# Kernel tuning notes

Hardware: AMD Instinct MI355X
Metric: run time of the kernel (lower is better)

## Reference

```python
import jax, jax.numpy as jnp
import numpy as np

B, T, F_IN, NF, K, H, NOUT = 512, 800, 3, 128, 15, 150, 10
EPS = 1e-5


def hard_sigmoid(x):
    # Keras-style hard sigmoid used by LSTMHardSigmoid gates
    return jnp.clip(0.2 * x + 0.5, 0.0, 1.0)


def adabn(x, gamma, beta, axes):
    # AdaBN: normalize with current-batch statistics, then learned affine.
    m = jnp.mean(x, axis=axes, keepdims=True)
    v = jnp.var(x, axis=axes, keepdims=True)
    shape = [1] * x.ndim
    shape[1] = x.shape[1]
    return (x - m) * jax.lax.rsqrt(v + EPS) * gamma.reshape(shape) + beta.reshape(shape)


def lstm_dir(x_tbf, w_ih, w_hh, b_ih, b_hh):
    # x_tbf: (T', B, F). PyTorch gate order i, f, g, o; hard-sigmoid gates.
    pre = jnp.einsum('tbf,gf->tbg', x_tbf, w_ih) + b_ih + b_hh  # (T', B, 4H)
    bsz = x_tbf.shape[1]
    h0 = jnp.zeros((bsz, H), x_tbf.dtype)
    c0 = jnp.zeros((bsz, H), x_tbf.dtype)

    def step(carry, pre_t):
        h, c = carry
        gates = pre_t + h @ w_hh.T
        i, f, g, o = jnp.split(gates, 4, axis=-1)
        i = hard_sigmoid(i)
        f = hard_sigmoid(f)
        o = hard_sigmoid(o)
        g = jnp.tanh(g)
        c = f * c + i * g
        h = o * jnp.tanh(c)
        return (h, c), h

    _, hs = jax.lax.scan(step, (h0, c0), pre)
    return hs  # (T', B, H)


def setup_inputs() -> dict:
    key = jax.random.key(0)
    ks = jax.random.split(key, 12)
    s = lambda i, shape, sc=0.05: jax.random.normal(ks[i], shape, jnp.float32) * sc
    G = 4 * H
    return {
        'x': jax.random.normal(ks[0], (B, F_IN, T), jnp.float32),
        'conv_w': s(1, (NF, F_IN, K)),
        'conv_b': jnp.zeros((NF,), jnp.float32),
        'bn1_g': jnp.ones((NF,), jnp.float32),
        'bn1_b': jnp.zeros((NF,), jnp.float32),
        'w_ih_f': s(2, (G, NF)), 'w_hh_f': s(3, (G, H)),
        'b_ih_f': jnp.zeros((G,), jnp.float32), 'b_hh_f': jnp.zeros((G,), jnp.float32),
        'w_ih_b': s(4, (G, NF)), 'w_hh_b': s(5, (G, H)),
        'b_ih_b': jnp.zeros((G,), jnp.float32), 'b_hh_b': jnp.zeros((G,), jnp.float32),
        'bn2_g': jnp.ones((2 * H,), jnp.float32), 'bn2_b': jnp.zeros((2 * H,), jnp.float32),
        'fc1_w': s(6, (50, 2 * H)), 'fc1_b': jnp.zeros((50,), jnp.float32),
        'bn3_g': jnp.ones((50,), jnp.float32), 'bn3_b': jnp.zeros((50,), jnp.float32),
        'fc2_w': s(7, (NOUT, 50)), 'fc2_b': jnp.zeros((NOUT,), jnp.float32),
    }


def reference(x, conv_w, conv_b, bn1_g, bn1_b,
              w_ih_f, w_hh_f, b_ih_f, b_hh_f,
              w_ih_b, w_hh_b, b_ih_b, b_hh_b,
              bn2_g, bn2_b, fc1_w, fc1_b, bn3_g, bn3_b, fc2_w, fc2_b):
    # net1: Conv1d(3->128, k=15) + ReLU + (Dropout=identity in eval) + MaxPool1d(2)
    y = jax.lax.conv_general_dilated(x, conv_w, (1,), 'VALID',
                                     dimension_numbers=('NCH', 'OIH', 'NCH'))
    y = jax.nn.relu(y + conv_b[None, :, None])  # (B, 128, 786)
    L = y.shape[2] // 2
    y = y[:, :, :2 * L].reshape(y.shape[0], NF, L, 2).max(-1)  # (B, 128, 393)
    # net1_adabn (per-channel over batch and time)
    y = adabn(y, bn1_g, bn1_b, axes=(0, 2))
    # net2: bidirectional hard-sigmoid LSTM, batch_first; zero initial states
    seq = jnp.transpose(y, (2, 0, 1))  # (393, B, 128)
    h_f = lstm_dir(seq, w_ih_f, w_hh_f, b_ih_f, b_hh_f)
    h_b = lstm_dir(seq[::-1], w_ih_b, w_hh_b, b_ih_b, b_hh_b)[::-1]
    h = jnp.concatenate([h_f, h_b], axis=-1)  # (393, B, 300)
    # global max-pool over time (F.max_pool1d with kernel = full length)
    pooled = h.max(axis=0)  # (B, 300)
    z = adabn(pooled, bn2_g, bn2_b, axes=(0,))
    z = jax.nn.relu(z @ fc1_w.T + fc1_b)  # (B, 50)
    z = adabn(z, bn3_g, bn3_b, axes=(0,))
    logits = z @ fc2_w.T + fc2_b  # (B, 10)
    return jax.nn.softmax(logits, axis=1)
```

## Files before the change

kernel.cpp:

```cpp
#include <hip/hip_runtime.h>
#include <math.h>

#define B_   512
#define T_   800
#define FIN  3
#define NF   128
#define KW   15
#define HID  150
#define LOUT 393
#define G4   600
#define NPAD 640
#define EPS  1e-5f

#define NT_  38
#define KT_  5
#define HSTR 152
#define PNT  40
#define PKT  4
#define PSTR 648

typedef _Float16 half8 __attribute__((ext_vector_type(8)));
typedef _Float16 half4 __attribute__((ext_vector_type(4)));
typedef float f32x4 __attribute__((ext_vector_type(4)));

__device__ __forceinline__ float hsig(float x){ return fminf(fmaxf(0.2f*x+0.5f,0.f),1.f); }
__device__ __forceinline__ float ftanh(float x){ float e=__expf(2.f*x); return 1.f - 2.f/(e+1.f); }

__global__ __launch_bounds__(512) void k_conv2(const float* __restrict__ x,
        const float* __restrict__ cw, const float* __restrict__ cb,
        _Float16* __restrict__ y16, float* __restrict__ st){
  __shared__ float xs[FIN][800];
  __shared__ float wl[NF*FIN*KW];
  __shared__ float rs[4][128], rq[4][128];
  int tid = threadIdx.x;
  int b = blockIdx.x;
  for (int i=tid;i<FIN*800;i+=512) (&xs[0][0])[i] = x[(size_t)b*(FIN*T_) + i];
  for (int i=tid;i<NF*FIN*KW;i+=512) wl[i]=cw[i];
  __syncthreads();
  int c = tid & 127, li = tid >> 7;
  float wr[FIN*KW];
  #pragma unroll
  for (int i=0;i<FIN*KW;i++) wr[i]=wl[c*FIN*KW+i];
  float cbv = cb[c];
  float s=0.f, q=0.f;
  for (int l=li; l<LOUT; l+=4){
    float a0=0.f, a1=0.f;
    #pragma unroll
    for (int f=0;f<FIN;f++){
      const float2* xp = (const float2*)&xs[f][0] + l;
      float xv[16];
      #pragma unroll
      for (int p=0;p<8;p++){ float2 v=xp[p]; xv[2*p]=v.x; xv[2*p+1]=v.y; }
      #pragma unroll
      for (int k=0;k<KW;k++){ float w=wr[f*KW+k]; a0 += w*xv[k]; a1 += w*xv[k+1]; }
    }
    float v = fmaxf(fmaxf(a0,a1)+cbv, 0.f);
    y16[((size_t)b*LOUT + l)*NF + c] = (_Float16)v;
    s += v; q += v*v;
  }
  rs[li][c]=s; rq[li][c]=q;
  __syncthreads();
  if (tid < 128){
    float ts = rs[0][c]+rs[1][c]+rs[2][c]+rs[3][c];
    float tq = rq[0][c]+rq[1][c]+rq[2][c]+rq[3][c];
    atomicAdd(&st[c], ts);
    atomicAdd(&st[128+c], tq);
  }
}

__global__ void k_prep_bias(const float* __restrict__ st,
    const float* __restrict__ g1, const float* __restrict__ b1v,
    const float* __restrict__ wf, const float* __restrict__ wb,
    const float* __restrict__ bif, const float* __restrict__ bhf,
    const float* __restrict__ bib, const float* __restrict__ bhb,
    float* __restrict__ bef, float* __restrict__ beb){
  int id = blockIdx.x*256 + threadIdx.x;
  if (id >= 2*NPAD) return;
  int dir = id/NPAD, g = id%NPAD;
  float* be = dir? beb : bef;
  if (g >= G4){ be[g]=0.f; return; }
  int src = (g&3)*HID + (g>>2);
  const float* wih = dir? wb : wf;
  float bias = dir? (bib[src]+bhb[src]) : (bif[src]+bhf[src]);
  const float Ninv = 1.f/((float)B_*(float)LOUT);
  for (int f=0;f<NF;f++){
    float m = st[f]*Ninv;
    float var = st[NF+f]*Ninv - m*m;
    float a = g1[f]*rsqrtf(var+EPS);
    float d = b1v[f] - m*a;
    bias += d*wih[(size_t)src*NF+f];
  }
  be[g] = bias;
}

__global__ void k_prep_wih(const float* __restrict__ st,
    const float* __restrict__ g1,
    const float* __restrict__ wf, const float* __restrict__ wb,
    _Float16* __restrict__ wT16){
  int id = blockIdx.x*256 + threadIdx.x;
  if (id >= 2*PNT*PKT*64) return;
  int lane = id & 63;
  int kt = (id>>6) & 3;
  int nt = (id>>8) % PNT;
  int dir = id / (PNT*PKT*64);
  const float* wih = dir? wb : wf;
  int n = nt*16 + (lane&15);
  int src = (n&3)*HID + (n>>2);
  int kb = kt*32 + (lane>>4)*8;
  const float Ninv = 1.f/((float)B_*(float)LOUT);
  half8 v;
  #pragma unroll
  for (int j=0;j<8;j++){
    int k = kb+j;
    float m = st[k]*Ninv;
    float var = st[NF+k]*Ninv - m*m;
    float a = g1[k]*rsqrtf(var+EPS);
    float f = (n < G4) ? wih[(size_t)src*NF + k]*a : 0.f;
    v[j] = (_Float16)f;
  }
  *(half8*)&wT16[(size_t)id*8] = v;
}

__global__ void k_prep_whh(const float* __restrict__ whf, const float* __restrict__ whb,
                           _Float16* __restrict__ wfrag){
  int id = blockIdx.x*256 + threadIdx.x;
  if (id >= 2*NT_*KT_*64) return;
  int lane = id & 63;
  int rest = id >> 6;
  int kt = rest % KT_;
  int nt = (rest/KT_) % NT_;
  int dir = rest / (KT_*NT_);
  const float* wh = dir? whb : whf;
  int n = nt*16 + (lane&15);
  int src = (n&3)*HID + (n>>2);
  int kb = kt*32 + (lane>>4)*8;
  half8 v;
  #pragma unroll
  for (int j=0;j<8;j++){
    int k = kb + j;
    float f = (n < G4 && k < HID) ? wh[(size_t)src*HID + k] : 0.f;
    v[j] = (_Float16)f;
  }
  *(half8*)&wfrag[(size_t)id*8] = v;
}

__global__ __launch_bounds__(1024)
void k_mega(const _Float16* __restrict__ wfrag,
            const _Float16* __restrict__ wT16,
            const float* __restrict__ bef, const float* __restrict__ beb,
            const _Float16* __restrict__ y16,
            const _Float16* __restrict__ prf, const _Float16* __restrict__ prb,
            _Float16* __restrict__ pwf, _Float16* __restrict__ pwb,
            float* __restrict__ hst, float* __restrict__ cst, float* __restrict__ mst,
            float* __restrict__ pooled,
            int nrec, int tc, int first, int last, int t0p){
  __shared__ __align__(16) _Float16 hh[2][16][168];
  __shared__ __align__(16) _Float16 pls[2][16][PSTR];
  int tid = threadIdx.x;
  int bid = blockIdx.x;

  if (bid < nrec){
    int dir = bid >> 5;
    int b0 = (bid & 31) * 16;
    const _Float16* pre = dir? prb : prf;
    int lane = tid & 63, w = tid >> 6;

    int cnt  = (w<6) ? 3 : 2;
    int base = (w<6) ? 3*w : 18 + 2*(w-6);
    const _Float16* wf = wfrag + (size_t)dir*NT_*KT_*64*8;
    half8 bfr[3][5];
    #pragma unroll
    for (int i=0;i<3;i++){
      #pragma unroll
      for (int kt=0;kt<KT_;kt++){
        int ntc = (i<cnt)? (base+i) : base;
        bfr[i][kt] = *(const half8*)&wf[(size_t)((ntc*KT_+kt)*64 + lane)*8];
      }
    }

    int batch = lane & 15;
    int uo[3]; bool uv[3];
    #pragma unroll
    for (int i=0;i<3;i++){
      uo[i] = (base+i)*4 + (lane>>4);
      uv[i] = (i<cnt) && (uo[i] < HID);
    }

    int srow0 = tid/80,        scol0 = (tid%80)*8;
    int srow1 = (tid+1024)/80, scol1 = ((tid+1024)%80)*8;
    bool s2 = tid < 256;

    for (int i=tid; i<2*16*168; i+=1024) (&hh[0][0][0])[i] = (_Float16)0.f;
    float c[3], m[3], hl[3];
    #pragma unroll
    for (int i=0;i<3;i++){ c[i]=0.f; m[i]=-1e30f; hl[i]=0.f; }
    __syncthreads();
    if (!first){
      #pragma unroll
      for (int i=0;i<3;i++){
        if (uv[i]){
          size_t gi = ((size_t)(dir*B_ + b0 + batch))*HSTR + uo[i];
          c[i]=cst[gi]; m[i]=mst[gi]; hl[i]=hst[gi];
          hh[0][batch][uo[i]] = (_Float16)hl[i];
        }
      }
    }
    {
      half8 s0 = *(const half8*)(pre + ((size_t)(b0 + srow0))*NPAD + scol0);
      *(half8*)&pls[0][srow0][scol0] = s0;
      if (s2){
        half8 s1 = *(const half8*)(pre + ((size_t)(b0 + srow1))*NPAD + scol1);
        *(half8*)&pls[0][srow1][scol1] = s1;
      }
    }
    __syncthreads();

    int cur = 0;
    for (int t=0; t<tc; t++){
      int nxt = cur ^ 1;
      half8 s0, s1;
      bool ld = (t+1 < tc);
      if (ld){
        size_t rbase = (size_t)(t+1)*B_ + b0;
        s0 = *(const half8*)(pre + (rbase + srow0)*NPAD + scol0);
        if (s2) s1 = *(const half8*)(pre + (rbase + srow1)*NPAD + scol1);
      }
      f32x4 acc0={0,0,0,0}, acc1={0,0,0,0}, acc2={0,0,0,0};
      #pragma unroll
      for (int kt=0; kt<KT_; kt++){
        half8 a = *(const half8*)&hh[cur][batch][kt*32 + (lane>>4)*8];
        acc0 = __builtin_amdgcn_mfma_f32_16x16x32_f16(bfr[0][kt], a, acc0, 0,0,0);
        acc1 = __builtin_amdgcn_mfma_f32_16x16x32_f16(bfr[1][kt], a, acc1, 0,0,0);
        if (cnt>2) acc2 = __builtin_amdgcn_mfma_f32_16x16x32_f16(bfr[2][kt], a, acc2, 0,0,0);
      }
      #define CELL(ACC, I)                                                     \
      if (uv[I]){                                                              \
        half4 pv = *(const half4*)&pls[cur][batch][4*uo[I]];                   \
        float xi = ACC[0] + (float)pv[0];                                      \
        float xf = ACC[1] + (float)pv[1];                                      \
        float xg = ACC[2] + (float)pv[2];                                      \
        float xo = ACC[3] + (float)pv[3];                                      \
        float ig=hsig(xi), fg=hsig(xf), og=hsig(xo), gg=ftanh(xg);             \
        c[I] = fg*c[I] + ig*gg;                                                \
        float hv = og*ftanh(c[I]);                                             \
        m[I] = fmaxf(m[I], hv);                                                \
        hl[I] = hv;                                                            \
        hh[nxt][batch][uo[I]] = (_Float16)hv;                                  \
      }
      CELL(acc0, 0)
      CELL(acc1, 1)
      CELL(acc2, 2)
      #undef CELL
      if (ld){
        *(half8*)&pls[nxt][srow0][scol0] = s0;
        if (s2) *(half8*)&pls[nxt][srow1][scol1] = s1;
      }
      __syncthreads();
      cur = nxt;
    }

    #pragma unroll
    for (int i=0;i<3;i++){
      if (uv[i]){
        size_t gi = ((size_t)(dir*B_ + b0 + batch))*HSTR + uo[i];
        cst[gi]=c[i]; mst[gi]=m[i]; hst[gi]=hl[i];
        if (last) pooled[(size_t)(b0+batch)*300 + dir*HID + uo[i]] = m[i];
      }
    }
    return;
  }

  {
    int pb = bid - nrec;
    int dir  = pb & 1;
    int t5   = pb >> 1;
    int by   = t5 % 5;
    int t2   = t5 / 5;
    int mb   = t2 & 1;
    int trel = t2 >> 1;
    const _Float16* wfp = wT16 + (size_t)dir*PNT*PKT*64*8;
    const float* be = dir? beb : bef;
    _Float16* pre = dir? pwb : pwf;
    int t = dir ? (LOUT-1-t0p-trel) : (t0p+trel);
    int n0 = by*128, nb = n0>>4;
    int lane = tid & 63, ww = tid >> 6;
    int m0 = mb*256 + ww*16;
    int arow = lane&15, aq = (lane>>4)*8;
    const _Float16* ap = y16 + ((size_t)(m0+arow)*LOUT + t)*NF + aq;
    f32x4 acc[8];
    #pragma unroll
    for (int j=0;j<8;j++) acc[j] = (f32x4){0,0,0,0};
    #pragma unroll
    for (int kt=0; kt<PKT; kt++){
      half8 a = *(const half8*)(ap + kt*32);
      #pragma unroll
      for (int nt=0; nt<8; nt++){
        half8 bf = *(const half8*)&wfp[(size_t)(((nb+nt)*PKT + kt)*64 + lane)*8];
        acc[nt] = __builtin_amdgcn_mfma_f32_16x16x32_f16(a, bf, acc[nt], 0,0,0);
      }
    }
    int dcol = lane&15, dq = (lane>>4)*4;
    size_t rowg = (size_t)trel*B_ + m0 + dq;
    #pragma unroll
    for (int nt=0; nt<8; nt++){
      int colL = n0 + nt*16 + dcol;
      float bv = be[colL];
      #pragma unroll
      for (int r=0;r<4;r++)
        pre[(rowg+r)*NPAD + colL] = (_Float16)(acc[nt][r] + bv);
    }
  }
}

__global__ void k_stats2(const float* __restrict__ pooled,
    const float* __restrict__ g2, const float* __restrict__ b2,
    float* __restrict__ a2, float* __restrict__ d2){
  int f = threadIdx.x;
  if (f >= 300) return;
  float s=0.f,q=0.f;
  for (int b=0;b<B_;b++){ float v = pooled[(size_t)b*300+f]; s+=v; q+=v*v; }
  float m = s*(1.f/B_), var = q*(1.f/B_) - m*m;
  float a = g2[f]*rsqrtf(var+EPS);
  a2[f]=a; d2[f]=b2[f]-m*a;
}

__global__ void k_fc1(const float* __restrict__ pooled,
    const float* __restrict__ a2, const float* __restrict__ d2,
    const float* __restrict__ w1, const float* __restrict__ fb1,
    float* __restrict__ z1){
  int o = blockIdx.x*256 + threadIdx.x;
  if (o >= B_*50) return;
  int b = o/50, j = o%50;
  float acc = fb1[j];
  for (int f=0;f<300;f++)
    acc += (a2[f]*pooled[(size_t)b*300+f] + d2[f]) * w1[j*300+f];
  z1[o] = fmaxf(acc,0.f);
}

__global__ void k_stats3(const float* __restrict__ z1,
    const float* __restrict__ g3, const float* __restrict__ b3,
    float* __restrict__ a3, float* __restrict__ d3){
  int f = threadIdx.x;
  if (f >= 50) return;
  float s=0.f,q=0.f;
  for (int b=0;b<B_;b++){ float v = z1[(size_t)b*50+f]; s+=v; q+=v*v; }
  float m = s*(1.f/B_), var = q*(1.f/B_) - m*m;
  float a = g3[f]*rsqrtf(var+EPS);
  a3[f]=a; d3[f]=b3[f]-m*a;
}

__global__ void k_fc2(const float* __restrict__ z1,
    const float* __restrict__ a3, const float* __restrict__ d3,
    const float* __restrict__ w2, const float* __restrict__ fb2,
    float* __restrict__ out){
  int b = blockIdx.x;
  int t = threadIdx.x;
  __shared__ float zl[50];
  __shared__ float lg[10];
  if (t<50) zl[t] = a3[t]*z1[(size_t)b*50+t] + d3[t];
  __syncthreads();
  if (t<10){
    float acc = fb2[t];
    for (int j=0;j<50;j++) acc += zl[j]*w2[t*50+j];
    lg[t]=acc;
  }
  __syncthreads();
  if (t<10){
    float m = lg[0];
    #pragma unroll
    for (int i=1;i<10;i++) m = fmaxf(m,lg[i]);
    float s = 0.f;
    #pragma unroll
    for (int i=0;i<10;i++) s += expf(lg[i]-m);
    out[(size_t)b*10+t] = expf(lg[t]-m)/s;
  }
}

extern "C" void kernel_launch(void* const* d_in, const int* in_sizes, int n_in,
                              void* d_out, int out_size, void* d_ws, size_t ws_size,
                              hipStream_t stream) {
  const float* x    = (const float*)d_in[0];
  const float* cw   = (const float*)d_in[1];
  const float* cb   = (const float*)d_in[2];
  const float* g1   = (const float*)d_in[3];
  const float* b1v  = (const float*)d_in[4];
  const float* wihf = (const float*)d_in[5];
  const float* whhf = (const float*)d_in[6];
  const float* bihf = (const float*)d_in[7];
  const float* bhhf = (const float*)d_in[8];
  const float* wihb = (const float*)d_in[9];
  const float* whhb = (const float*)d_in[10];
  const float* bihb = (const float*)d_in[11];
  const float* bhhb = (const float*)d_in[12];
  const float* g2   = (const float*)d_in[13];
  const float* b2   = (const float*)d_in[14];
  const float* w1   = (const float*)d_in[15];
  const float* fb1  = (const float*)d_in[16];
  const float* g3   = (const float*)d_in[17];
  const float* b3   = (const float*)d_in[18];
  const float* w2   = (const float*)d_in[19];
  const float* fb2  = (const float*)d_in[20];
  float* out = (float*)d_out;

  uint8_t* base = (uint8_t*)d_ws;
  size_t off = 0;
  auto allocB = [&](size_t nbytes)->uint8_t*{
    uint8_t* p = base + off;
    off = (off + nbytes + 255) & ~(size_t)255;
    return p;
  };
  _Float16* y16   = (_Float16*)allocB((size_t)B_*LOUT*NF*2);
  float* st       = (float*)allocB(256*4);
  _Float16* wT16  = (_Float16*)allocB((size_t)2*PNT*PKT*64*8*2);
  float* bef      = (float*)allocB(NPAD*4);
  float* beb      = (float*)allocB(NPAD*4);
  _Float16* wfrag = (_Float16*)allocB((size_t)2*NT_*KT_*64*8*2);
  float* hst      = (float*)allocB((size_t)2*B_*HSTR*4);
  float* cst      = (float*)allocB((size_t)2*B_*HSTR*4);
  float* mst      = (float*)allocB((size_t)2*B_*HSTR*4);
  float* pooled   = (float*)allocB((size_t)B_*300*4);
  float* a2       = (float*)allocB(320*4);
  float* d2       = (float*)allocB(320*4);
  float* z1       = (float*)allocB((size_t)B_*50*4);
  float* a3       = (float*)allocB(64*4);
  float* d3       = (float*)allocB(64*4);
  size_t fixedEnd = off;

  size_t avail = (ws_size > fixedEnd + 4096) ? (ws_size - fixedEnd - 4096) : 0;
  size_t per_t1 = (size_t)2*B_*NPAD*2;
  size_t per_t2 = (size_t)4*B_*NPAD*2;
  int nch, TC;
  if (avail / per_t1 >= (size_t)LOUT){
    nch = 1; TC = LOUT;
  } else {
    int tcmax = (int)(avail / per_t2);
    if (tcmax < 1) tcmax = 1;
    if (tcmax > LOUT) tcmax = LOUT;
    nch = (LOUT + tcmax - 1) / tcmax;
    TC = (LOUT + nch - 1) / nch;
  }
  _Float16* preA_f = (_Float16*)allocB((size_t)TC*B_*NPAD*2);
  _Float16* preA_b = (_Float16*)allocB((size_t)TC*B_*NPAD*2);
  _Float16* preB_f = preA_f;
  _Float16* preB_b = preA_b;
  if (nch > 1){
    preB_f = (_Float16*)allocB((size_t)TC*B_*NPAD*2);
    preB_b = (_Float16*)allocB((size_t)TC*B_*NPAD*2);
  }
  auto t0of = [&](int k){ return k*TC; };
  auto tcof = [&](int k){ int r = LOUT - k*TC; return (r < TC) ? r : TC; };

  hipMemsetAsync(st, 0, 256*4, stream);
  k_conv2<<<B_, 512, 0, stream>>>(x, cw, cb, y16, st);
  k_prep_bias<<<(2*NPAD+255)/256, 256, 0, stream>>>(st, g1, b1v, wihf, wihb,
                                                    bihf, bhhf, bihb, bhhb, bef, beb);
  k_prep_wih<<<(2*PNT*PKT*64+255)/256, 256, 0, stream>>>(st, g1, wihf, wihb, wT16);
  k_prep_whh<<<(2*NT_*KT_*64+255)/256, 256, 0, stream>>>(whhf, whhb, wfrag);

  k_mega<<<tcof(0)*20, 1024, 0, stream>>>(wfrag, wT16, bef, beb, y16,
      preA_f, preA_b, preA_f, preA_b, hst, cst, mst, pooled,
      0, 0, 0, 0, t0of(0));
  for (int k=0; k<nch; k++){
    int hasN = (k+1 < nch) ? 1 : 0;
    _Float16* rf = (k & 1) ? preB_f : preA_f;
    _Float16* rb = (k & 1) ? preB_b : preA_b;
    _Float16* wf_ = ((k+1) & 1) ? preB_f : preA_f;
    _Float16* wb_ = ((k+1) & 1) ? preB_b : preA_b;
    int grid = 64 + (hasN ? tcof(k+1)*20 : 0);
    k_mega<<<grid, 1024, 0, stream>>>(wfrag, wT16, bef, beb, y16,
        rf, rb, wf_, wb_, hst, cst, mst, pooled,
        64, tcof(k), (k==0) ? 1 : 0, hasN ? 0 : 1, hasN ? t0of(k+1) : 0);
  }

  k_stats2<<<1, 320, 0, stream>>>(pooled, g2, b2, a2, d2);
  k_fc1<<<(B_*50+255)/256, 256, 0, stream>>>(pooled, a2, d2, w1, fb1, z1);
  k_stats3<<<1, 64, 0, stream>>>(z1, g3, b3, a3, d3);
  k_fc2<<<B_, 64, 0, stream>>>(z1, a3, d3, w2, fb2, out);
}
```

Baseline: 895.1 us.

## Split LSTM recurrence across 128 blocks, register-block conv, parallelize BN stats

```diff
diff --git a/kernel.cpp b/kernel.cpp
--- a/kernel.cpp
+++ b/kernel.cpp
@@ -26,15 +26,17 @@
 __device__ __forceinline__ float hsig(float x){ return fminf(fmaxf(0.2f*x+0.5f,0.f),1.f); }
 __device__ __forceinline__ float ftanh(float x){ float e=__expf(2.f*x); return 1.f - 2.f/(e+1.f); }
 
-__global__ __launch_bounds__(512) void k_conv2(const float* __restrict__ x,
+__global__ __launch_bounds__(512) void k_conv3(const float* __restrict__ x,
         const float* __restrict__ cw, const float* __restrict__ cb,
         _Float16* __restrict__ y16, float* __restrict__ st){
-  __shared__ float xs[FIN][800];
+  __shared__ __align__(16) float xs[FIN][808];
   __shared__ float wl[NF*FIN*KW];
   __shared__ float rs[4][128], rq[4][128];
   int tid = threadIdx.x;
   int b = blockIdx.x;
-  for (int i=tid;i<FIN*800;i+=512) (&xs[0][0])[i] = x[(size_t)b*(FIN*T_) + i];
+  for (int i=tid;i<FIN*800;i+=512){ int f=i/800, p=i-f*800;
+    xs[f][p] = x[(size_t)b*(FIN*T_) + i]; }
+  if (tid < FIN*8){ int f=tid/8, p=800+(tid&7); xs[f][p]=0.f; }
   for (int i=tid;i<NF*FIN*KW;i+=512) wl[i]=cw[i];
   __syncthreads();
   int c = tid & 127, li = tid >> 7;
@@ -43,20 +45,37 @@
   for (int i=0;i<FIN*KW;i++) wr[i]=wl[c*FIN*KW+i];
   float cbv = cb[c];
   float s=0.f, q=0.f;
-  for (int l=li; l<LOUT; l+=4){
-    float a0=0.f, a1=0.f;
+  int l0 = li*100;
+  int lend = (l0+100 < LOUT) ? l0+100 : LOUT;
+  for (int l4=l0; l4<lend; l4+=4){
+    float a0[4]={0,0,0,0}, a1[4]={0,0,0,0};
     #pragma unroll
     for (int f=0;f<FIN;f++){
-      const float2* xp = (const float2*)&xs[f][0] + l;
-      float xv[16];
-      #pragma unroll
-      for (int p=0;p<8;p++){ float2 v=xp[p]; xv[2*p]=v.x; xv[2*p+1]=v.y; }
-      #pragma unroll
-      for (int k=0;k<KW;k++){ float w=wr[f*KW+k]; a0 += w*xv[k]; a1 += w*xv[k+1]; }
-    }
-    float v = fmaxf(fmaxf(a0,a1)+cbv, 0.f);
-    y16[((size_t)b*LOUT + l)*NF + c] = (_Float16)v;
-    s += v; q += v*v;
+      float xw[24];
+      #pragma unroll
+      for (int j=0;j<6;j++){
+        float4 v = *(const float4*)&xs[f][2*l4 + 4*j];
+        xw[4*j+0]=v.x; xw[4*j+1]=v.y; xw[4*j+2]=v.z; xw[4*j+3]=v.w;
+      }
+      #pragma unroll
+      for (int dl=0; dl<4; dl++){
+        #pragma unroll
+        for (int k=0;k<KW;k++){
+          float wv = wr[f*KW+k];
+          a0[dl] += wv*xw[2*dl+k];
+          a1[dl] += wv*xw[2*dl+k+1];
+        }
+      }
+    }
+    #pragma unroll
+    for (int dl=0; dl<4; dl++){
+      int l = l4+dl;
+      if (l < lend){
+        float v = fmaxf(fmaxf(a0[dl],a1[dl])+cbv, 0.f);
+        y16[((size_t)b*LOUT + l)*NF + c] = (_Float16)v;
+        s += v; q += v*v;
+      }
+    }
   }
   rs[li][c]=s; rq[li][c]=q;
   __syncthreads();
@@ -144,7 +163,7 @@
   *(half8*)&wfrag[(size_t)id*8] = v;
 }
 
-__global__ __launch_bounds__(1024)
+__global__ __launch_bounds__(512)
 void k_mega(const _Float16* __restrict__ wfrag,
             const _Float16* __restrict__ wT16,
             const float* __restrict__ bef, const float* __restrict__ beb,
@@ -152,52 +171,52 @@
             const _Float16* __restrict__ prf, const _Float16* __restrict__ prb,
             _Float16* __restrict__ pwf, _Float16* __restrict__ pwb,
             float* __restrict__ hst, float* __restrict__ cst, float* __restrict__ mst,
-            float* __restrict__ pooled,
+            float* __restrict__ pooledT,
             int nrec, int tc, int first, int last, int t0p){
-  __shared__ __align__(16) _Float16 hh[2][16][168];
-  __shared__ __align__(16) _Float16 pls[2][16][PSTR];
+  __shared__ __align__(16) _Float16 hh[2][8][168];
+  __shared__ __align__(16) _Float16 pls[2][8][PSTR];
   int tid = threadIdx.x;
   int bid = blockIdx.x;
 
   if (bid < nrec){
-    int dir = bid >> 5;
-    int b0 = (bid & 31) * 16;
+    int dir = bid >> 6;
+    int b0 = (bid & 63) * 8;
     const _Float16* pre = dir? prb : prf;
     int lane = tid & 63, w = tid >> 6;
 
-    int cnt  = (w<6) ? 3 : 2;
-    int base = (w<6) ? 3*w : 18 + 2*(w-6);
+    int cnt  = (w<6) ? 5 : 4;
+    int base = (w<6) ? 5*w : 30 + 4*(w-6);
     const _Float16* wf = wfrag + (size_t)dir*NT_*KT_*64*8;
-    half8 bfr[3][5];
-    #pragma unroll
-    for (int i=0;i<3;i++){
-      #pragma unroll
-      for (int kt=0;kt<KT_;kt++){
-        int ntc = (i<cnt)? (base+i) : base;
+    half8 bfr[5][5];
+    #pragma unroll
+    for (int i=0;i<5;i++){
+      int ntc = (i<cnt)? (base+i) : base;
+      #pragma unroll
+      for (int kt=0;kt<KT_;kt++)
         bfr[i][kt] = *(const half8*)&wf[(size_t)((ntc*KT_+kt)*64 + lane)*8];
-      }
     }
 
     int batch = lane & 15;
-    int uo[3]; bool uv[3];
-    #pragma unroll
-    for (int i=0;i<3;i++){
+    int brow = batch & 7;
+    int uo[5]; bool uv[5];
+    #pragma unroll
+    for (int i=0;i<5;i++){
       uo[i] = (base+i)*4 + (lane>>4);
-      uv[i] = (i<cnt) && (uo[i] < HID);
+      uv[i] = (i<cnt) && (uo[i] < HID) && (batch < 8);
     }
 
     int srow0 = tid/80,        scol0 = (tid%80)*8;
-    int srow1 = (tid+1024)/80, scol1 = ((tid+1024)%80)*8;
-    bool s2 = tid < 256;
-
-    for (int i=tid; i<2*16*168; i+=1024) (&hh[0][0][0])[i] = (_Float16)0.f;
-    float c[3], m[3], hl[3];
-    #pragma unroll
-    for (int i=0;i<3;i++){ c[i]=0.f; m[i]=-1e30f; hl[i]=0.f; }
+    int srow1 = (tid+512)/80,  scol1 = ((tid+512)%80)*8;
+    bool s2 = tid < 128;
+
+    for (int i=tid; i<2*8*168; i+=512) (&hh[0][0][0])[i] = (_Float16)0.f;
+    float c[5], m[5], hl[5];
+    #pragma unroll
+    for (int i=0;i<5;i++){ c[i]=0.f; m[i]=-1e30f; hl[i]=0.f; }
     __syncthreads();
     if (!first){
       #pragma unroll
-      for (int i=0;i<3;i++){
+      for (int i=0;i<5;i++){
         if (uv[i]){
           size_t gi = ((size_t)(dir*B_ + b0 + batch))*HSTR + uo[i];
           c[i]=cst[gi]; m[i]=mst[gi]; hl[i]=hst[gi];
@@ -225,13 +244,15 @@
         s0 = *(const half8*)(pre + (rbase + srow0)*NPAD + scol0);
         if (s2) s1 = *(const half8*)(pre + (rbase + srow1)*NPAD + scol1);
       }
-      f32x4 acc0={0,0,0,0}, acc1={0,0,0,0}, acc2={0,0,0,0};
+      f32x4 acc0={0,0,0,0}, acc1={0,0,0,0}, acc2={0,0,0,0}, acc3={0,0,0,0}, acc4={0,0,0,0};
       #pragma unroll
       for (int kt=0; kt<KT_; kt++){
-        half8 a = *(const half8*)&hh[cur][batch][kt*32 + (lane>>4)*8];
+        half8 a = *(const half8*)&hh[cur][brow][kt*32 + (lane>>4)*8];
         acc0 = __builtin_amdgcn_mfma_f32_16x16x32_f16(bfr[0][kt], a, acc0, 0,0,0);
         acc1 = __builtin_amdgcn_mfma_f32_16x16x32_f16(bfr[1][kt], a, acc1, 0,0,0);
-        if (cnt>2) acc2 = __builtin_amdgcn_mfma_f32_16x16x32_f16(bfr[2][kt], a, acc2, 0,0,0);
+        acc2 = __builtin_amdgcn_mfma_f32_16x16x32_f16(bfr[2][kt], a, acc2, 0,0,0);
+        acc3 = __builtin_amdgcn_mfma_f32_16x16x32_f16(bfr[3][kt], a, acc3, 0,0,0);
+        if (cnt>4) acc4 = __builtin_amdgcn_mfma_f32_16x16x32_f16(bfr[4][kt], a, acc4, 0,0,0);
       }
       #define CELL(ACC, I)                                                     \
       if (uv[I]){                                                              \
@@ -250,6 +271,8 @@
       CELL(acc0, 0)
       CELL(acc1, 1)
       CELL(acc2, 2)
+      CELL(acc3, 3)
+      CELL(acc4, 4)
       #undef CELL
       if (ld){
         *(half8*)&pls[nxt][srow0][scol0] = s0;
@@ -260,11 +283,11 @@
     }
 
     #pragma unroll
-    for (int i=0;i<3;i++){
+    for (int i=0;i<5;i++){
       if (uv[i]){
         size_t gi = ((size_t)(dir*B_ + b0 + batch))*HSTR + uo[i];
         cst[gi]=c[i]; mst[gi]=m[i]; hst[gi]=hl[i];
-        if (last) pooled[(size_t)(b0+batch)*300 + dir*HID + uo[i]] = m[i];
+        if (last) pooledT[(size_t)(dir*HID + uo[i])*512 + b0 + batch] = m[i];
       }
     }
     return;
@@ -275,16 +298,16 @@
     int dir  = pb & 1;
     int t5   = pb >> 1;
     int by   = t5 % 5;
-    int t2   = t5 / 5;
-    int mb   = t2 & 1;
-    int trel = t2 >> 1;
+    int t4   = t5 / 5;
+    int mb   = t4 & 3;
+    int trel = t4 >> 2;
     const _Float16* wfp = wT16 + (size_t)dir*PNT*PKT*64*8;
     const float* be = dir? beb : bef;
     _Float16* pre = dir? pwb : pwf;
     int t = dir ? (LOUT-1-t0p-trel) : (t0p+trel);
     int n0 = by*128, nb = n0>>4;
     int lane = tid & 63, ww = tid >> 6;
-    int m0 = mb*256 + ww*16;
+    int m0 = mb*128 + ww*16;
     int arow = lane&15, aq = (lane>>4)*8;
     const _Float16* ap = y16 + ((size_t)(m0+arow)*LOUT + t)*NF + aq;
     f32x4 acc[8];
@@ -312,19 +335,30 @@
   }
 }
 
-__global__ void k_stats2(const float* __restrict__ pooled,
+__global__ __launch_bounds__(256) void k_stats2(const float* __restrict__ pooledT,
     const float* __restrict__ g2, const float* __restrict__ b2,
     float* __restrict__ a2, float* __restrict__ d2){
-  int f = threadIdx.x;
-  if (f >= 300) return;
-  float s=0.f,q=0.f;
-  for (int b=0;b<B_;b++){ float v = pooled[(size_t)b*300+f]; s+=v; q+=v*v; }
-  float m = s*(1.f/B_), var = q*(1.f/B_) - m*m;
-  float a = g2[f]*rsqrtf(var+EPS);
-  a2[f]=a; d2[f]=b2[f]-m*a;
-}
-
-__global__ void k_fc1(const float* __restrict__ pooled,
+  int f = blockIdx.x;
+  int t = threadIdx.x;
+  float v1 = pooledT[(size_t)f*512 + t];
+  float v2 = pooledT[(size_t)f*512 + 256 + t];
+  float s = v1+v2, q = v1*v1+v2*v2;
+  #pragma unroll
+  for (int off=1; off<64; off<<=1){ s += __shfl_xor(s,off); q += __shfl_xor(q,off); }
+  __shared__ float ls[4], lq[4];
+  int lane = t & 63, w = t >> 6;
+  if (lane==0){ ls[w]=s; lq[w]=q; }
+  __syncthreads();
+  if (t==0){
+    s = ls[0]+ls[1]+ls[2]+ls[3];
+    q = lq[0]+lq[1]+lq[2]+lq[3];
+    float m = s*(1.f/B_), var = q*(1.f/B_) - m*m;
+    float a = g2[f]*rsqrtf(var+EPS);
+    a2[f]=a; d2[f]=b2[f]-m*a;
+  }
+}
+
+__global__ void k_fc1(const float* __restrict__ pooledT,
     const float* __restrict__ a2, const float* __restrict__ d2,
     const float* __restrict__ w1, const float* __restrict__ fb1,
     float* __restrict__ z1){
@@ -333,20 +367,25 @@
   int b = o/50, j = o%50;
   float acc = fb1[j];
   for (int f=0;f<300;f++)
-    acc += (a2[f]*pooled[(size_t)b*300+f] + d2[f]) * w1[j*300+f];
+    acc += (a2[f]*pooledT[(size_t)f*512 + b] + d2[f]) * w1[j*300+f];
   z1[o] = fmaxf(acc,0.f);
 }
 
-__global__ void k_stats3(const float* __restrict__ z1,
+__global__ __launch_bounds__(64) void k_stats3(const float* __restrict__ z1,
     const float* __restrict__ g3, const float* __restrict__ b3,
     float* __restrict__ a3, float* __restrict__ d3){
-  int f = threadIdx.x;
-  if (f >= 50) return;
+  int f = blockIdx.x;
+  int t = threadIdx.x;
   float s=0.f,q=0.f;
-  for (int b=0;b<B_;b++){ float v = z1[(size_t)b*50+f]; s+=v; q+=v*v; }
-  float m = s*(1.f/B_), var = q*(1.f/B_) - m*m;
-  float a = g3[f]*rsqrtf(var+EPS);
-  a3[f]=a; d3[f]=b3[f]-m*a;
+  #pragma unroll
+  for (int k=0;k<8;k++){ float v = z1[(size_t)(t + 64*k)*50 + f]; s+=v; q+=v*v; }
+  #pragma unroll
+  for (int off=1; off<64; off<<=1){ s += __shfl_xor(s,off); q += __shfl_xor(q,off); }
+  if (t==0){
+    float m = s*(1.f/B_), var = q*(1.f/B_) - m*m;
+    float a = g3[f]*rsqrtf(var+EPS);
+    a3[f]=a; d3[f]=b3[f]-m*a;
+  }
 }
 
 __global__ void k_fc2(const float* __restrict__ z1,
@@ -409,21 +448,21 @@
     off = (off + nbytes + 255) & ~(size_t)255;
     return p;
   };
-  _Float16* y16   = (_Float16*)allocB((size_t)B_*LOUT*NF*2);
-  float* st       = (float*)allocB(256*4);
-  _Float16* wT16  = (_Float16*)allocB((size_t)2*PNT*PKT*64*8*2);
-  float* bef      = (float*)allocB(NPAD*4);
-  float* beb      = (float*)allocB(NPAD*4);
-  _Float16* wfrag = (_Float16*)allocB((size_t)2*NT_*KT_*64*8*2);
-  float* hst      = (float*)allocB((size_t)2*B_*HSTR*4);
-  float* cst      = (float*)allocB((size_t)2*B_*HSTR*4);
-  float* mst      = (float*)allocB((size_t)2*B_*HSTR*4);
-  float* pooled   = (float*)allocB((size_t)B_*300*4);
-  float* a2       = (float*)allocB(320*4);
-  float* d2       = (float*)allocB(320*4);
-  float* z1       = (float*)allocB((size_t)B_*50*4);
-  float* a3       = (float*)allocB(64*4);
-  float* d3       = (float*)allocB(64*4);
+  _Float16* y16    = (_Float16*)allocB((size_t)B_*LOUT*NF*2);
+  float* st        = (float*)allocB(256*4);
+  _Float16* wT16   = (_Float16*)allocB((size_t)2*PNT*PKT*64*8*2);
+  float* bef       = (float*)allocB(NPAD*4);
+  float* beb       = (float*)allocB(NPAD*4);
+  _Float16* wfrag  = (_Float16*)allocB((size_t)2*NT_*KT_*64*8*2);
+  float* hst       = (float*)allocB((size_t)2*B_*HSTR*4);
+  float* cst       = (float*)allocB((size_t)2*B_*HSTR*4);
+  float* mst       = (float*)allocB((size_t)2*B_*HSTR*4);
+  float* pooledT   = (float*)allocB((size_t)300*512*4);
+  float* a2        = (float*)allocB(320*4);
+  float* d2        = (float*)allocB(320*4);
+  float* z1        = (float*)allocB((size_t)B_*50*4);
+  float* a3        = (float*)allocB(64*4);
+  float* d3        = (float*)allocB(64*4);
   size_t fixedEnd = off;
 
   size_t avail = (ws_size > fixedEnd + 4096) ? (ws_size - fixedEnd - 4096) : 0;
@@ -451,14 +490,14 @@
   auto tcof = [&](int k){ int r = LOUT - k*TC; return (r < TC) ? r : TC; };
 
   hipMemsetAsync(st, 0, 256*4, stream);
-  k_conv2<<<B_, 512, 0, stream>>>(x, cw, cb, y16, st);
+  k_conv3<<<B_, 512, 0, stream>>>(x, cw, cb, y16, st);
   k_prep_bias<<<(2*NPAD+255)/256, 256, 0, stream>>>(st, g1, b1v, wihf, wihb,
                                                     bihf, bhhf, bihb, bhhb, bef, beb);
   k_prep_wih<<<(2*PNT*PKT*64+255)/256, 256, 0, stream>>>(st, g1, wihf, wihb, wT16);
   k_prep_whh<<<(2*NT_*KT_*64+255)/256, 256, 0, stream>>>(whhf, whhb, wfrag);
 
-  k_mega<<<tcof(0)*20, 1024, 0, stream>>>(wfrag, wT16, bef, beb, y16,
-      preA_f, preA_b, preA_f, preA_b, hst, cst, mst, pooled,
+  k_mega<<<tcof(0)*40, 512, 0, stream>>>(wfrag, wT16, bef, beb, y16,
+      preA_f, preA_b, preA_f, preA_b, hst, cst, mst, pooledT,
       0, 0, 0, 0, t0of(0));
   for (int k=0; k<nch; k++){
     int hasN = (k+1 < nch) ? 1 : 0;
@@ -466,14 +505,14 @@
     _Float16* rb = (k & 1) ? preB_b : preA_b;
     _Float16* wf_ = ((k+1) & 1) ? preB_f : preA_f;
     _Float16* wb_ = ((k+1) & 1) ? preB_b : preA_b;
-    int grid = 64 + (hasN ? tcof(k+1)*20 : 0);
-    k_mega<<<grid, 1024, 0, stream>>>(wfrag, wT16, bef, beb, y16,
-        rf, rb, wf_, wb_, hst, cst, mst, pooled,
-        64, tcof(k), (k==0) ? 1 : 0, hasN ? 0 : 1, hasN ? t0of(k+1) : 0);
-  }
-
-  k_stats2<<<1, 320, 0, stream>>>(pooled, g2, b2, a2, d2);
-  k_fc1<<<(B_*50+255)/256, 256, 0, stream>>>(pooled, a2, d2, w1, fb1, z1);
-  k_stats3<<<1, 64, 0, stream>>>(z1, g3, b3, a3, d3);
+    int grid = 128 + (hasN ? tcof(k+1)*40 : 0);
+    k_mega<<<grid, 512, 0, stream>>>(wfrag, wT16, bef, beb, y16,
+        rf, rb, wf_, wb_, hst, cst, mst, pooledT,
+        128, tcof(k), (k==0) ? 1 : 0, hasN ? 0 : 1, hasN ? t0of(k+1) : 0);
+  }
+
+  k_stats2<<<300, 256, 0, stream>>>(pooledT, g2, b2, a2, d2);
+  k_fc1<<<(B_*50+255)/256, 256, 0, stream>>>(pooledT, a2, d2, w1, fb1, z1);
+  k_stats3<<<50, 64, 0, stream>>>(z1, g3, b3, a3, d3);
   k_fc2<<<B_, 64, 0, stream>>>(z1, a3, d3, w2, fb2, out);
 }
```

Result: no change. 888.3 us (-0.8%).
